# Kernel optimization log

Measured on AMD Instinct MI355X. Metric: run time of the kernel, lower is better.

The kernel has to match this reference:

```python
import jax, jax.numpy as jnp
import numpy as np

EPS = 1e-5  # torch group_norm default
GROUPS = 32


def _nin(t, W, b):
    # torch Nin: einsum('bchw,co->bowh') transposes spatial dims, then adds bias
    return jnp.einsum('bchw,co->bowh', t, W) + b


def setup_inputs() -> dict:
    key = jax.random.key(0)
    ks = jax.random.split(key, 9)
    B, C, N = 16, 512, 32
    x = jax.random.normal(ks[0], (B, C, N, N), jnp.float32)
    sc = 0.02
    Wq = jax.random.normal(ks[1], (C, C), jnp.float32) * sc
    Wk = jax.random.normal(ks[2], (C, C), jnp.float32) * sc
    Wv = jax.random.normal(ks[3], (C, C), jnp.float32) * sc
    Wn = jax.random.normal(ks[4], (C, C), jnp.float32) * sc
    bq = jnp.zeros((1, C, 1, 1), jnp.float32)
    bk = jnp.zeros((1, C, 1, 1), jnp.float32)
    bv = jnp.zeros((1, C, 1, 1), jnp.float32)
    bn = jnp.zeros((1, C, 1, 1), jnp.float32)
    return {"x": x, "Wq": Wq, "bq": bq, "Wk": Wk, "bk": bk,
            "Wv": Wv, "bv": bv, "Wn": Wn, "bn": bn}


def reference(x, Wq, bq, Wk, bk, Wv, bv, Wn, bn):
    B, C, H, W = x.shape
    # GroupNorm(32) with no affine params
    xg = x.reshape(B, GROUPS, -1)
    mu = xg.mean(-1, keepdims=True)
    var = xg.var(-1, keepdims=True)
    h = ((xg - mu) / jnp.sqrt(var + EPS)).reshape(B, C, H, W)
    # Nin projections -> spatially transposed (B, C, W, H)
    q = _nin(h, Wq, bq)
    k = _nin(h, Wk, bk)
    v = _nin(h, Wv, bv)
    # scores s[b,w1,w2,h1,h2] = sum_c q[b,c,w1,h1] k[b,c,w2,h2] * C^-0.5
    s = jnp.einsum('bcwh,bcWH->bwWhH', q, k) * (C ** -0.5)
    # softmax over flat (h1,h2) blocks exactly as the torch reshape does
    s = jax.nn.softmax(s.reshape(B, H, W, H * W), axis=-1).reshape(B, H, W, H, W)
    # torch.einsum('bHWHW, bcWH -> bcWH', w, v) takes the DIAGONAL over the
    # repeated H and W labels: diag[b,i,j] = s[b,i,j,i,j], then elementwise
    # scales v: out[b,c,w,h] = diag[b,h,w] * v[b,c,w,h]
    i = jnp.arange(H)
    j = jnp.arange(W)
    diag = s[:, i[:, None], j[None, :], i[:, None], j[None, :]]  # (B,H,W)
    h2 = v * jnp.swapaxes(diag, 1, 2)[:, None]  # (B,C,W,H)
    out = _nin(h2, Wn, bn)  # transposes back -> (B,C,H,W)
    return x + out
```

## Files before the change

### kernel.cpp

```cpp
#include <hip/hip_runtime.h>
#include <hip/hip_bf16.h>

typedef __attribute__((ext_vector_type(8))) short short8;
typedef __attribute__((ext_vector_type(4))) float floatx4;

#define MFMA16(a, b, c) __builtin_amdgcn_mfma_f32_16x16x32_bf16((a), (b), (c), 0, 0, 0)
#define WAIT_VM(N) asm volatile("s_waitcnt vmcnt(" #N ")" ::: "memory")
#define BAR() __builtin_amdgcn_s_barrier()

__device__ __forceinline__ short f2bf(float f) {
    union { float f; unsigned u; } x; x.f = f;
    unsigned r = (x.u + 0x7fffu + ((x.u >> 16) & 1u)) >> 16;
    return (short)r;
}

__device__ __forceinline__ void gl2lds16(const short* g, short* l) {
    void* gv = const_cast<short*>(g);
    __builtin_amdgcn_global_load_lds((__attribute__((address_space(1))) void*)gv,
                                     (__attribute__((address_space(3))) void*)l,
                                     16, 0, 0);
}

__global__ void transpose_w4(const float* __restrict__ Wq, const float* __restrict__ Wk,
                             const float* __restrict__ Wv, const float* __restrict__ Wn,
                             const float* __restrict__ bq, const float* __restrict__ bk,
                             const float* __restrict__ bv,
                             short* __restrict__ Wqkv_t, short* __restrict__ Wn_t,
                             float* __restrict__ bias_cat) {
    __shared__ float t[32][33];
    int z = blockIdx.z;
    const float* Wsrc = (z == 0) ? Wq : (z == 1) ? Wk : (z == 2) ? Wv : Wn;
    int o0 = blockIdx.x * 32, c0 = blockIdx.y * 32;
    int lx = threadIdx.x, ly = threadIdx.y;
    for (int i = ly; i < 32; i += 8) t[i][lx] = Wsrc[(size_t)(c0 + i) * 512 + o0 + lx];
    __syncthreads();
    for (int i = ly; i < 32; i += 8) {
        short v = f2bf(t[lx][i]);
        if (z < 3) Wqkv_t[(size_t)(z * 512 + o0 + i) * 512 + c0 + lx] = v;
        else       Wn_t[(size_t)(o0 + i) * 512 + c0 + lx] = v;
    }
    if (z < 3 && blockIdx.y == 0 && ly == 0) {
        const float* bsrc = (z == 0) ? bq : (z == 1) ? bk : bv;
        bias_cat[z * 512 + o0 + lx] = bsrc[o0 + lx];
    }
}

__global__ __launch_bounds__(256) void groupnorm_k(const float* __restrict__ x,
                                                   short* __restrict__ hnt) {
    int b = blockIdx.x >> 5, g = blockIdx.x & 31;
    const float* xg = x + ((size_t)b * 512 + g * 16) * 1024;
    const float4* xg4 = (const float4*)xg;
    float s = 0.f, ss = 0.f;
    for (int i = threadIdx.x; i < 4096; i += 256) {
        float4 v = xg4[i];
        s  += v.x + v.y + v.z + v.w;
        ss += v.x * v.x + v.y * v.y + v.z * v.z + v.w * v.w;
    }
#pragma unroll
    for (int off = 32; off > 0; off >>= 1) {
        s  += __shfl_down(s,  off, 64);
        ss += __shfl_down(ss, off, 64);
    }
    __shared__ float red[8];
    int w = threadIdx.x >> 6;
    if ((threadIdx.x & 63) == 0) { red[w] = s; red[4 + w] = ss; }
    __syncthreads();
    float S  = red[0] + red[1] + red[2] + red[3];
    float SS = red[4] + red[5] + red[6] + red[7];
    float mean = S * (1.f / 16384.f);
    float var  = SS * (1.f / 16384.f) - mean * mean;
    float rstd = rsqrtf(var + 1e-5f);
    __shared__ __attribute__((aligned(16))) short tile[16 * 1026];
    for (int i = threadIdx.x; i < 4096; i += 256) {
        float4 v = xg4[i];
        int c = i >> 8, p = (i & 255) * 4;
        short* tp = tile + c * 1026 + p;
        tp[0] = f2bf((v.x - mean) * rstd);
        tp[1] = f2bf((v.y - mean) * rstd);
        tp[2] = f2bf((v.z - mean) * rstd);
        tp[3] = f2bf((v.w - mean) * rstd);
    }
    __syncthreads();
    for (int i = threadIdx.x; i < 2048; i += 256) {
        int p = i >> 1, half = i & 1;
        short8 v;
#pragma unroll
        for (int j = 0; j < 8; ++j) v[j] = tile[(half * 8 + j) * 1026 + p];
        *(short8*)(hnt + ((size_t)b * 1024 + p) * 512 + g * 16 + half * 8) = v;
    }
}

__global__ __launch_bounds__(256) void qkv_gemm(const short* __restrict__ A,
                                                const short* __restrict__ Wt,
                                                const float* __restrict__ bias_cat,
                                                short* __restrict__ Qp,
                                                short* __restrict__ Kp,
                                                short* __restrict__ Vb) {
    const int tid = threadIdx.x;
    const int wv = tid >> 6, ln = tid & 63;
    const int fid = blockIdx.x + (blockIdx.y << 3) + blockIdx.z * 96;
    const int xcd = fid & 7, slot = fid >> 3;
    const int bb = (slot >= 96) ? 1 : 0;
    const int w = slot - bb * 96;
    const int batch = xcd * 2 + bb;
    const int m0 = (w & 7) * 128, n0 = (w >> 3) * 128;
    const size_t BS = 1024 * 512;
    const short* Ab = A + (size_t)batch * BS;
    const int tsel = n0 >> 9;
    const int permute = (tsel < 2);
    short* Ob = ((tsel == 0) ? Qp : (tsel == 1) ? Kp : Vb) + (size_t)batch * BS;

    __shared__ __attribute__((aligned(16))) short As[3][128 * 32];
    __shared__ __attribute__((aligned(16))) short Bs[3][128 * 32];

    floatx4 acc[4][4] = {};
    const int wm = (wv >> 1) * 64, wn = (wv & 1) * 64;
    const int fr = ln & 15, fq = ln >> 4;

    int sr[2], sq[2];
#pragma unroll
    for (int j = 0; j < 2; ++j) {
        int s = (wv * 2 + j) * 64 + ln;
        sr[j] = s >> 2;
        sq[j] = ((s & 3) ^ ((sr[j] >> 1) & 3)) * 8;
    }
    int aoff[4], boff[4];
#pragma unroll
    for (int t = 0; t < 4; ++t) {
        int ra = wm + t * 16 + fr;
        aoff[t] = ra * 32 + ((fq ^ ((ra >> 1) & 3)) * 8);
        int rb = wn + t * 16 + fr;
        boff[t] = rb * 32 + ((fq ^ ((rb >> 1) & 3)) * 8);
    }

    short* a0 = &As[0][0]; short* a1 = &As[1][0]; short* a2 = &As[2][0];
    short* b0 = &Bs[0][0]; short* b1 = &Bs[1][0]; short* b2 = &Bs[2][0];

#pragma unroll
    for (int j = 0; j < 2; ++j) {
        gl2lds16(Ab + (size_t)(m0 + sr[j]) * 512 + sq[j],      a0 + (wv * 2 + j) * 512);
        gl2lds16(Wt + (size_t)(n0 + sr[j]) * 512 + sq[j],      b0 + (wv * 2 + j) * 512);
        gl2lds16(Ab + (size_t)(m0 + sr[j]) * 512 + 32 + sq[j], a1 + (wv * 2 + j) * 512);
        gl2lds16(Wt + (size_t)(n0 + sr[j]) * 512 + 32 + sq[j], b1 + (wv * 2 + j) * 512);
    }

    auto compute = [&](const short* Ap, const short* Bp) {
        short8 af[4], bfr[4];
#pragma unroll
        for (int t = 0; t < 4; ++t) {
            af[t]  = *(const short8*)(Ap + aoff[t]);
            bfr[t] = *(const short8*)(Bp + boff[t]);
        }
#pragma unroll
        for (int mt = 0; mt < 4; ++mt)
#pragma unroll
            for (int nt = 0; nt < 4; ++nt)
                acc[mt][nt] = MFMA16(af[mt], bfr[nt], acc[mt][nt]);
    };

    for (int t = 0; t < 14; ++t) {
        int kp = t * 32 + 64;
#pragma unroll
        for (int j = 0; j < 2; ++j) {
            gl2lds16(Ab + (size_t)(m0 + sr[j]) * 512 + kp + sq[j], a2 + (wv * 2 + j) * 512);
            gl2lds16(Wt + (size_t)(n0 + sr[j]) * 512 + kp + sq[j], b2 + (wv * 2 + j) * 512);
        }
        WAIT_VM(8);
        BAR();
        compute(a0, b0);
        BAR();
        short* ta = a0; a0 = a1; a1 = a2; a2 = ta;
        short* tb = b0; b0 = b1; b1 = b2; b2 = tb;
    }
    WAIT_VM(4); BAR();
    compute(a0, b0);
    WAIT_VM(0); BAR();
    compute(a1, b1);

#pragma unroll
    for (int mt = 0; mt < 4; ++mt) {
#pragma unroll
        for (int nt = 0; nt < 4; ++nt) {
            int n = n0 + wn + nt * 16 + fr;
            float bvv = bias_cat[n];
            int nn = n & 511;
#pragma unroll
            for (int r = 0; r < 4; ++r) {
                int m = m0 + wm + mt * 16 + fq * 4 + r;
                int mrow = permute ? ((m & 31) * 32 + (m >> 5)) : m;
                Ob[(size_t)mrow * 512 + nn] = f2bf(acc[mt][nt][r] + bvv);
            }
        }
    }
}

__global__ __launch_bounds__(256, 2) void attn_sm(const short* __restrict__ Qp,
                                                  const short* __restrict__ Kp,
                                                  float* __restrict__ Dm) {
    const int tid = threadIdx.x;
    const int wv = tid >> 6, ln = tid & 63;
    const int fid = blockIdx.x + (blockIdx.y << 3) + blockIdx.z * 32;
    const int xcd = fid & 7, slot = fid >> 3;
    const int bb = (slot >= 32) ? 1 : 0;
    const int w = slot - bb * 32;
    const int b = xcd * 2 + bb;
    const int m0 = (w & 7) * 128, n0 = (w >> 3) * 256;
    const short* Qb = Qp + (size_t)b * (1024 * 512);
    const short* Kb = Kp + (size_t)b * (1024 * 512);

    __shared__ __attribute__((aligned(16))) short As[3][128 * 32];
    __shared__ __attribute__((aligned(16))) short Bs[3][256 * 32];

    floatx4 acc[4][8] = {};
    const int wm = (wv >> 1) * 64, wn = (wv & 1) * 128;
    const int fr = ln & 15, fq = ln >> 4;

    int ar[2], aq[2], br[4], bq_[4];
#pragma unroll
    for (int j = 0; j < 2; ++j) {
        int s = (wv * 2 + j) * 64 + ln;
        ar[j] = s >> 2;
        aq[j] = ((s & 3) ^ ((ar[j] >> 1) & 3)) * 8;
    }
#pragma unroll
    for (int j = 0; j < 4; ++j) {
        int s = (wv * 4 + j) * 64 + ln;
        br[j] = s >> 2;
        bq_[j] = ((s & 3) ^ ((br[j] >> 1) & 3)) * 8;
    }
    int aoff[4], boff[8];
#pragma unroll
    for (int t = 0; t < 4; ++t) {
        int ra = wm + t * 16 + fr;
        aoff[t] = ra * 32 + ((fq ^ ((ra >> 1) & 3)) * 8);
    }
#pragma unroll
    for (int u = 0; u < 8; ++u) {
        int rb = wn + u * 16 + fr;
        boff[u] = rb * 32 + ((fq ^ ((rb >> 1) & 3)) * 8);
    }

    short* a0 = &As[0][0]; short* a1 = &As[1][0]; short* a2 = &As[2][0];
    short* b0 = &Bs[0][0]; short* b1 = &Bs[1][0]; short* b2 = &Bs[2][0];

#pragma unroll
    for (int j = 0; j < 2; ++j) {
        gl2lds16(Qb + (size_t)(m0 + ar[j]) * 512 + aq[j],      a0 + (wv * 2 + j) * 512);
        gl2lds16(Qb + (size_t)(m0 + ar[j]) * 512 + 32 + aq[j], a1 + (wv * 2 + j) * 512);
    }
#pragma unroll
    for (int j = 0; j < 4; ++j) {
        gl2lds16(Kb + (size_t)(n0 + br[j]) * 512 + bq_[j],      b0 + (wv * 4 + j) * 512);
        gl2lds16(Kb + (size_t)(n0 + br[j]) * 512 + 32 + bq_[j], b1 + (wv * 4 + j) * 512);
    }

    auto compute = [&](const short* Ap, const short* Bp) {
        short8 af[4], bfr[8];
#pragma unroll
        for (int t = 0; t < 4; ++t) af[t] = *(const short8*)(Ap + aoff[t]);
#pragma unroll
        for (int u = 0; u < 8; ++u) bfr[u] = *(const short8*)(Bp + boff[u]);
#pragma unroll
        for (int mt = 0; mt < 4; ++mt)
#pragma unroll
            for (int nt = 0; nt < 8; ++nt)
                acc[mt][nt] = MFMA16(af[mt], bfr[nt], acc[mt][nt]);
    };

    for (int t = 0; t < 14; ++t) {
        int kp = t * 32 + 64;
#pragma unroll
        for (int j = 0; j < 2; ++j)
            gl2lds16(Qb + (size_t)(m0 + ar[j]) * 512 + kp + aq[j], a2 + (wv * 2 + j) * 512);
#pragma unroll
        for (int j = 0; j < 4; ++j)
            gl2lds16(Kb + (size_t)(n0 + br[j]) * 512 + kp + bq_[j], b2 + (wv * 4 + j) * 512);
        WAIT_VM(12);
        BAR();
        compute(a0, b0);
        BAR();
        short* ta = a0; a0 = a1; a1 = a2; a2 = ta;
        short* tb = b0; b0 = b1; b1 = b2; b2 = tb;
    }
    WAIT_VM(6); BAR();
    compute(a0, b0);
    WAIT_VM(0); BAR();
    compute(a1, b1);

    const float scale = 0.04419417382415922f;
    const int wbase = (m0 + wm) >> 5;
    const int Wbase = (n0 + wn) >> 5;
#pragma unroll
    for (int si = 0; si < 2; ++si) {
#pragma unroll
        for (int sj = 0; sj < 4; ++sj) {
            int wg = wbase + si, Wg = Wbase + sj;
            float tv[16];
            float mx = -3.0e38f;
#pragma unroll
            for (int mi = 0; mi < 2; ++mi)
#pragma unroll
                for (int ni = 0; ni < 2; ++ni)
#pragma unroll
                    for (int r = 0; r < 4; ++r) {
                        float u = acc[2 * si + mi][2 * sj + ni][r] * scale;
                        tv[(mi * 2 + ni) * 4 + r] = u;
                        mx = fmaxf(mx, u);
                    }
#pragma unroll
            for (int off = 32; off > 0; off >>= 1) mx = fmaxf(mx, __shfl_xor(mx, off, 64));
            float se = 0.f;
#pragma unroll
            for (int i = 0; i < 16; ++i) se += __expf(tv[i] - mx);
#pragma unroll
            for (int off = 32; off > 0; off >>= 1) se += __shfl_xor(se, off, 64);
            if (fq == ((wg >> 2) & 3) && fr == (Wg & 15)) {
                int mi = wg >> 4, ni = Wg >> 4;
                float numer = tv[(mi * 2 + ni) * 4 + (wg & 3)];
                Dm[((size_t)b * 32 + wg) * 32 + Wg] = __expf(numer - mx) / se;
            }
        }
    }
}

__global__ __launch_bounds__(256) void out_gemm(const short* __restrict__ A,
                                                const short* __restrict__ Wt,
                                                const float* __restrict__ Dm,
                                                const float* __restrict__ bnb,
                                                const float* __restrict__ x,
                                                float* __restrict__ out) {
    const int tid = threadIdx.x;
    const int wv = tid >> 6, ln = tid & 63;
    const int fid = blockIdx.x + (blockIdx.y << 3) + blockIdx.z * 32;
    const int xcd = fid & 7, slot = fid >> 3;
    const int bb = (slot >= 32) ? 1 : 0;
    const int w = slot - bb * 32;
    const int b = xcd * 2 + bb;
    const int m0 = (w & 7) * 128, n0 = (w >> 3) * 128;
    const size_t BS = 1024 * 512;
    const short* Ab = A + (size_t)b * BS;

    __shared__ __attribute__((aligned(16))) short As[3][128 * 32];
    __shared__ __attribute__((aligned(16))) short Bs[3][128 * 32];

    floatx4 acc[4][4] = {};
    const int wm = (wv >> 1) * 64, wn = (wv & 1) * 64;
    const int fr = ln & 15, fq = ln >> 4;

    int sr[2], sq[2];
#pragma unroll
    for (int j = 0; j < 2; ++j) {
        int s = (wv * 2 + j) * 64 + ln;
        sr[j] = s >> 2;
        sq[j] = ((s & 3) ^ ((sr[j] >> 1) & 3)) * 8;
    }
    int aoff[4], boff[4];
#pragma unroll
    for (int t = 0; t < 4; ++t) {
        int ra = wm + t * 16 + fr;
        aoff[t] = ra * 32 + ((fq ^ ((ra >> 1) & 3)) * 8);
        int rb = wn + t * 16 + fr;
        boff[t] = rb * 32 + ((fq ^ ((rb >> 1) & 3)) * 8);
    }

    short* a0 = &As[0][0]; short* a1 = &As[1][0]; short* a2 = &As[2][0];
    short* b0 = &Bs[0][0]; short* b1 = &Bs[1][0]; short* b2 = &Bs[2][0];

#pragma unroll
    for (int j = 0; j < 2; ++j) {
        gl2lds16(Ab + (size_t)(m0 + sr[j]) * 512 + sq[j],      a0 + (wv * 2 + j) * 512);
        gl2lds16(Wt + (size_t)(n0 + sr[j]) * 512 + sq[j],      b0 + (wv * 2 + j) * 512);
        gl2lds16(Ab + (size_t)(m0 + sr[j]) * 512 + 32 + sq[j], a1 + (wv * 2 + j) * 512);
        gl2lds16(Wt + (size_t)(n0 + sr[j]) * 512 + 32 + sq[j], b1 + (wv * 2 + j) * 512);
    }

    auto compute = [&](const short* Ap, const short* Bp) {
        short8 af[4], bfr[4];
#pragma unroll
        for (int t = 0; t < 4; ++t) {
            af[t]  = *(const short8*)(Ap + aoff[t]);
            bfr[t] = *(const short8*)(Bp + boff[t]);
        }
#pragma unroll
        for (int mt = 0; mt < 4; ++mt)
#pragma unroll
            for (int nt = 0; nt < 4; ++nt)
                acc[mt][nt] = MFMA16(af[mt], bfr[nt], acc[mt][nt]);
    };

    for (int t = 0; t < 14; ++t) {
        int kp = t * 32 + 64;
#pragma unroll
        for (int j = 0; j < 2; ++j) {
            gl2lds16(Ab + (size_t)(m0 + sr[j]) * 512 + kp + sq[j], a2 + (wv * 2 + j) * 512);
            gl2lds16(Wt + (size_t)(n0 + sr[j]) * 512 + kp + sq[j], b2 + (wv * 2 + j) * 512);
        }
        WAIT_VM(8);
        BAR();
        compute(a0, b0);
        BAR();
        short* ta = a0; a0 = a1; a1 = a2; a2 = ta;
        short* tb = b0; b0 = b1; b1 = b2; b2 = tb;
    }
    WAIT_VM(4); BAR();
    compute(a0, b0);
    WAIT_VM(0); BAR();
    compute(a1, b1);

#pragma unroll
    for (int mt = 0; mt < 4; ++mt) {
        int mbase = m0 + wm + mt * 16 + fq * 4;
        float4 d4 = *(const float4*)(Dm + (size_t)b * 1024 + mbase);
#pragma unroll
        for (int nt = 0; nt < 4; ++nt) {
            int n = n0 + wn + nt * 16 + fr;
            float bvv = bnb[n];
            size_t base = ((size_t)b * 512 + n) * 1024 + mbase;
            float4 x4 = *(const float4*)(x + base);
            float4 o;
            o.x = x4.x + d4.x * acc[mt][nt][0] + bvv;
            o.y = x4.y + d4.y * acc[mt][nt][1] + bvv;
            o.z = x4.z + d4.z * acc[mt][nt][2] + bvv;
            o.w = x4.w + d4.w * acc[mt][nt][3] + bvv;
            *(float4*)(out + base) = o;
        }
    }
}

extern "C" void kernel_launch(void* const* d_in, const int* in_sizes, int n_in,
                              void* d_out, int out_size, void* d_ws, size_t ws_size,
                              hipStream_t stream) {
    const float* x  = (const float*)d_in[0];
    const float* Wq = (const float*)d_in[1];
    const float* bq = (const float*)d_in[2];
    const float* Wk = (const float*)d_in[3];
    const float* bk = (const float*)d_in[4];
    const float* Wv = (const float*)d_in[5];
    const float* bv = (const float*)d_in[6];
    const float* Wn = (const float*)d_in[7];
    const float* bn = (const float*)d_in[8];
    float* out = (float*)d_out;
    char* ws = (char*)d_ws;

    const size_t WQKV = (size_t)1536 * 512 * 2;
    const size_t WSZ  = (size_t)512 * 512 * 2;
    const size_t BIAS = 1536 * sizeof(float);
    const size_t TSZ  = (size_t)16 * 1024 * 512 * 2;
    short* Wqkv_t   = (short*)(ws);
    short* Wn_t     = (short*)(ws + WQKV);
    float* bias_cat = (float*)(ws + WQKV + WSZ);
    char*  base     = ws + WQKV + WSZ + BIAS;
    short* hnt = (short*)(base);
    short* Qp  = (short*)(base + TSZ);
    short* Kp  = (short*)(base + 2 * TSZ);
    short* Vb  = (short*)(base + 3 * TSZ);
    float* Dm  = (float*)(base + 4 * TSZ);

    transpose_w4<<<dim3(16, 16, 4), dim3(32, 8), 0, stream>>>(
        Wq, Wk, Wv, Wn, bq, bk, bv, Wqkv_t, Wn_t, bias_cat);
    groupnorm_k<<<512, 256, 0, stream>>>(x, hnt);
    qkv_gemm<<<dim3(8, 12, 16), 256, 0, stream>>>(hnt, Wqkv_t, bias_cat, Qp, Kp, Vb);
    attn_sm<<<dim3(8, 4, 16), 256, 0, stream>>>(Qp, Kp, Dm);
    out_gemm<<<dim3(8, 4, 16), 256, 0, stream>>>(Vb, Wn_t, Dm, bn, x, out);
}
```

Measured before the change: 201.4 us.

## Fold Q/K and V/out projections into precomputed weight products

Replaces the three per-batch QKV projections with algebraically folded weight products: G = Wq·Wk^T so scores become h·G·h^T plus rank-one bias terms, and W2 = Wv·Wn so the output GEMM reads normalized activations directly. Bias contributions are precomputed as vectors (u, v, c, Wn^T·bv) and applied in the attention and output epilogues. This cuts the per-batch GEMM work from three projections to one and drops the Q/K/V buffers. In exchange it adds small weight-only GEMM and prep kernels plus extra bf16 rounding of the fused weight products.

```diff
diff --git a/kernel.cpp b/kernel.cpp
--- a/kernel.cpp
+++ b/kernel.cpp
@@ -13,6 +13,10 @@
     unsigned r = (x.u + 0x7fffu + ((x.u >> 16) & 1u)) >> 16;
     return (short)r;
 }
+__device__ __forceinline__ float b2f(short s) {
+    union { unsigned u; float f; } x; x.u = ((unsigned)(unsigned short)s) << 16; return x.f;
+}
+__device__ __forceinline__ int swap5(int p) { return ((p & 31) << 5) | (p >> 5); }
 
 __device__ __forceinline__ void gl2lds16(const short* g, short* l) {
     void* gv = const_cast<short*>(g);
@@ -21,28 +25,140 @@
                                      16, 0, 0);
 }
 
-__global__ void transpose_w4(const float* __restrict__ Wq, const float* __restrict__ Wk,
-                             const float* __restrict__ Wv, const float* __restrict__ Wn,
-                             const float* __restrict__ bq, const float* __restrict__ bk,
-                             const float* __restrict__ bv,
-                             short* __restrict__ Wqkv_t, short* __restrict__ Wn_t,
-                             float* __restrict__ bias_cat) {
+__global__ void prep_w(const float* __restrict__ Wq, const float* __restrict__ Wk,
+                       const float* __restrict__ Wv, const float* __restrict__ Wn,
+                       short* __restrict__ Wqc, short* __restrict__ Wkc,
+                       short* __restrict__ Wvc, short* __restrict__ Wnt) {
     __shared__ float t[32][33];
     int z = blockIdx.z;
-    const float* Wsrc = (z == 0) ? Wq : (z == 1) ? Wk : (z == 2) ? Wv : Wn;
     int o0 = blockIdx.x * 32, c0 = blockIdx.y * 32;
     int lx = threadIdx.x, ly = threadIdx.y;
-    for (int i = ly; i < 32; i += 8) t[i][lx] = Wsrc[(size_t)(c0 + i) * 512 + o0 + lx];
-    __syncthreads();
-    for (int i = ly; i < 32; i += 8) {
-        short v = f2bf(t[lx][i]);
-        if (z < 3) Wqkv_t[(size_t)(z * 512 + o0 + i) * 512 + c0 + lx] = v;
-        else       Wn_t[(size_t)(o0 + i) * 512 + c0 + lx] = v;
-    }
-    if (z < 3 && blockIdx.y == 0 && ly == 0) {
-        const float* bsrc = (z == 0) ? bq : (z == 1) ? bk : bv;
-        bias_cat[z * 512 + o0 + lx] = bsrc[o0 + lx];
-    }
+    if (z < 3) {
+        const float* src = (z == 0) ? Wq : (z == 1) ? Wk : Wv;
+        short* dst = (z == 0) ? Wqc : (z == 1) ? Wkc : Wvc;
+        for (int i = ly; i < 32; i += 8) {
+            size_t idx = (size_t)(c0 + i) * 512 + o0 + lx;
+            dst[idx] = f2bf(src[idx]);
+        }
+    } else {
+        for (int i = ly; i < 32; i += 8) t[i][lx] = Wn[(size_t)(c0 + i) * 512 + o0 + lx];
+        __syncthreads();
+        for (int i = ly; i < 32; i += 8)
+            Wnt[(size_t)(o0 + i) * 512 + c0 + lx] = f2bf(t[lx][i]);
+    }
+}
+
+__global__ void prep_uv(const float* __restrict__ Wq, const float* __restrict__ Wk,
+                        const float* __restrict__ Wn, const float* __restrict__ bq,
+                        const float* __restrict__ bk, const float* __restrict__ bv,
+                        float* __restrict__ UVC) {
+    int t = threadIdx.x;
+    float u = 0.f, v = 0.f, w2 = 0.f;
+    for (int o = 0; o < 512; ++o) {
+        u  += Wq[(size_t)t * 512 + o] * bk[o];
+        v  += Wk[(size_t)t * 512 + o] * bq[o];
+        w2 += bv[o] * Wn[(size_t)o * 512 + t];
+    }
+    UVC[t] = u; UVC[512 + t] = v; UVC[1025 + t] = w2;
+    if (t == 0) {
+        float c = 0.f;
+        for (int o = 0; o < 512; ++o) c += bq[o] * bk[o];
+        UVC[1024] = c;
+    }
+}
+
+__global__ __launch_bounds__(256) void gemm2(const short* __restrict__ Wkc,
+                                             const short* __restrict__ Wqc,
+                                             const short* __restrict__ Wnt,
+                                             const short* __restrict__ Wvc,
+                                             short* __restrict__ Gt,
+                                             short* __restrict__ W2t) {
+    const int tid = threadIdx.x;
+    const int wv = tid >> 6, ln = tid & 63;
+    const int z = blockIdx.y;
+    const short* A  = (z == 0) ? Wkc : Wnt;
+    const short* Wt = (z == 0) ? Wqc : Wvc;
+    short* O = (z == 0) ? Gt : W2t;
+    const int m0 = (blockIdx.x & 3) * 128, n0 = (blockIdx.x >> 2) * 128;
+
+    __shared__ __attribute__((aligned(16))) short As[3][128 * 32];
+    __shared__ __attribute__((aligned(16))) short Bs[3][128 * 32];
+
+    floatx4 acc[4][4] = {};
+    const int wm = (wv >> 1) * 64, wn = (wv & 1) * 64;
+    const int fr = ln & 15, fq = ln >> 4;
+
+    int sr[2], sq[2];
+#pragma unroll
+    for (int j = 0; j < 2; ++j) {
+        int s = (wv * 2 + j) * 64 + ln;
+        sr[j] = s >> 2;
+        sq[j] = ((s & 3) ^ ((sr[j] >> 1) & 3)) * 8;
+    }
+    int aoff[4], boff[4];
+#pragma unroll
+    for (int t = 0; t < 4; ++t) {
+        int ra = wm + t * 16 + fr;
+        aoff[t] = ra * 32 + ((fq ^ ((ra >> 1) & 3)) * 8);
+        int rb = wn + t * 16 + fr;
+        boff[t] = rb * 32 + ((fq ^ ((rb >> 1) & 3)) * 8);
+    }
+
+    short* a0 = &As[0][0]; short* a1 = &As[1][0]; short* a2 = &As[2][0];
+    short* b0 = &Bs[0][0]; short* b1 = &Bs[1][0]; short* b2 = &Bs[2][0];
+
+#pragma unroll
+    for (int j = 0; j < 2; ++j) {
+        gl2lds16(A  + (size_t)(m0 + sr[j]) * 512 + sq[j],      a0 + (wv * 2 + j) * 512);
+        gl2lds16(Wt + (size_t)(n0 + sr[j]) * 512 + sq[j],      b0 + (wv * 2 + j) * 512);
+        gl2lds16(A  + (size_t)(m0 + sr[j]) * 512 + 32 + sq[j], a1 + (wv * 2 + j) * 512);
+        gl2lds16(Wt + (size_t)(n0 + sr[j]) * 512 + 32 + sq[j], b1 + (wv * 2 + j) * 512);
+    }
+
+    auto compute = [&](const short* Ap, const short* Bp) {
+        short8 af[4], bfr[4];
+#pragma unroll
+        for (int t = 0; t < 4; ++t) {
+            af[t]  = *(const short8*)(Ap + aoff[t]);
+            bfr[t] = *(const short8*)(Bp + boff[t]);
+        }
+#pragma unroll
+        for (int mt = 0; mt < 4; ++mt)
+#pragma unroll
+            for (int nt = 0; nt < 4; ++nt)
+                acc[mt][nt] = MFMA16(af[mt], bfr[nt], acc[mt][nt]);
+    };
+
+    for (int t = 0; t < 14; ++t) {
+        int kp = t * 32 + 64;
+#pragma unroll
+        for (int j = 0; j < 2; ++j) {
+            gl2lds16(A  + (size_t)(m0 + sr[j]) * 512 + kp + sq[j], a2 + (wv * 2 + j) * 512);
+            gl2lds16(Wt + (size_t)(n0 + sr[j]) * 512 + kp + sq[j], b2 + (wv * 2 + j) * 512);
+        }
+        WAIT_VM(8);
+        BAR();
+        compute(a0, b0);
+        BAR();
+        short* ta = a0; a0 = a1; a1 = a2; a2 = ta;
+        short* tb = b0; b0 = b1; b1 = b2; b2 = tb;
+    }
+    WAIT_VM(4); BAR();
+    compute(a0, b0);
+    WAIT_VM(0); BAR();
+    compute(a1, b1);
+
+#pragma unroll
+    for (int mt = 0; mt < 4; ++mt)
+#pragma unroll
+        for (int nt = 0; nt < 4; ++nt) {
+            int n = n0 + wn + nt * 16 + fr;
+#pragma unroll
+            for (int r = 0; r < 4; ++r) {
+                int m = m0 + wm + mt * 16 + fq * 4 + r;
+                O[(size_t)m * 512 + n] = f2bf(acc[mt][nt][r]);
+            }
+        }
 }
 
 __global__ __launch_bounds__(256) void groupnorm_k(const float* __restrict__ x,
@@ -90,25 +206,48 @@
     }
 }
 
-__global__ __launch_bounds__(256) void qkv_gemm(const short* __restrict__ A,
-                                                const short* __restrict__ Wt,
-                                                const float* __restrict__ bias_cat,
-                                                short* __restrict__ Qp,
-                                                short* __restrict__ Kp,
-                                                short* __restrict__ Vb) {
+__global__ __launch_bounds__(256) void ruv_k(const short* __restrict__ hnt,
+                                             const float* __restrict__ UVC,
+                                             float* __restrict__ RuP,
+                                             float* __restrict__ RvP) {
+    const int b = blockIdx.x >> 4, part = blockIdx.x & 15;
+    const int wv = threadIdx.x >> 6, ln = threadIdx.x & 63;
+    float uc[8], vc[8];
+#pragma unroll
+    for (int j = 0; j < 8; ++j) { uc[j] = UVC[ln * 8 + j]; vc[j] = UVC[512 + ln * 8 + j]; }
+    for (int rr = 0; rr < 16; ++rr) {
+        int p = part * 64 + wv * 16 + rr;
+        short8 h = *(const short8*)(hnt + ((size_t)b * 1024 + p) * 512 + ln * 8);
+        float su = 0.f, sv = 0.f;
+#pragma unroll
+        for (int j = 0; j < 8; ++j) { float hv = b2f(h[j]); su += hv * uc[j]; sv += hv * vc[j]; }
+#pragma unroll
+        for (int off = 32; off > 0; off >>= 1) {
+            su += __shfl_xor(su, off, 64);
+            sv += __shfl_xor(sv, off, 64);
+        }
+        if (ln == 0) {
+            int pp = swap5(p);
+            RuP[(size_t)b * 1024 + pp] = su;
+            RvP[(size_t)b * 1024 + pp] = sv;
+        }
+    }
+}
+
+__global__ __launch_bounds__(256) void tgemm(const short* __restrict__ A,
+                                             const short* __restrict__ Gt,
+                                             short* __restrict__ Tp) {
     const int tid = threadIdx.x;
     const int wv = tid >> 6, ln = tid & 63;
-    const int fid = blockIdx.x + (blockIdx.y << 3) + blockIdx.z * 96;
+    const int fid = blockIdx.x;
     const int xcd = fid & 7, slot = fid >> 3;
-    const int bb = (slot >= 96) ? 1 : 0;
-    const int w = slot - bb * 96;
+    const int bb = (slot >= 32) ? 1 : 0;
+    const int w = slot - bb * 32;
     const int batch = xcd * 2 + bb;
     const int m0 = (w & 7) * 128, n0 = (w >> 3) * 128;
     const size_t BS = 1024 * 512;
     const short* Ab = A + (size_t)batch * BS;
-    const int tsel = n0 >> 9;
-    const int permute = (tsel < 2);
-    short* Ob = ((tsel == 0) ? Qp : (tsel == 1) ? Kp : Vb) + (size_t)batch * BS;
+    short* Ob = Tp + (size_t)batch * BS;
 
     __shared__ __attribute__((aligned(16))) short As[3][128 * 32];
     __shared__ __attribute__((aligned(16))) short Bs[3][128 * 32];
@@ -139,9 +278,9 @@
 #pragma unroll
     for (int j = 0; j < 2; ++j) {
         gl2lds16(Ab + (size_t)(m0 + sr[j]) * 512 + sq[j],      a0 + (wv * 2 + j) * 512);
-        gl2lds16(Wt + (size_t)(n0 + sr[j]) * 512 + sq[j],      b0 + (wv * 2 + j) * 512);
+        gl2lds16(Gt + (size_t)(n0 + sr[j]) * 512 + sq[j],      b0 + (wv * 2 + j) * 512);
         gl2lds16(Ab + (size_t)(m0 + sr[j]) * 512 + 32 + sq[j], a1 + (wv * 2 + j) * 512);
-        gl2lds16(Wt + (size_t)(n0 + sr[j]) * 512 + 32 + sq[j], b1 + (wv * 2 + j) * 512);
+        gl2lds16(Gt + (size_t)(n0 + sr[j]) * 512 + 32 + sq[j], b1 + (wv * 2 + j) * 512);
     }
 
     auto compute = [&](const short* Ap, const short* Bp) {
@@ -163,7 +302,7 @@
 #pragma unroll
         for (int j = 0; j < 2; ++j) {
             gl2lds16(Ab + (size_t)(m0 + sr[j]) * 512 + kp + sq[j], a2 + (wv * 2 + j) * 512);
-            gl2lds16(Wt + (size_t)(n0 + sr[j]) * 512 + kp + sq[j], b2 + (wv * 2 + j) * 512);
+            gl2lds16(Gt + (size_t)(n0 + sr[j]) * 512 + kp + sq[j], b2 + (wv * 2 + j) * 512);
         }
         WAIT_VM(8);
         BAR();
@@ -178,24 +317,23 @@
     compute(a1, b1);
 
 #pragma unroll
-    for (int mt = 0; mt < 4; ++mt) {
+    for (int mt = 0; mt < 4; ++mt)
 #pragma unroll
         for (int nt = 0; nt < 4; ++nt) {
             int n = n0 + wn + nt * 16 + fr;
-            float bvv = bias_cat[n];
-            int nn = n & 511;
 #pragma unroll
             for (int r = 0; r < 4; ++r) {
                 int m = m0 + wm + mt * 16 + fq * 4 + r;
-                int mrow = permute ? ((m & 31) * 32 + (m >> 5)) : m;
-                Ob[(size_t)mrow * 512 + nn] = f2bf(acc[mt][nt][r] + bvv);
+                Ob[(size_t)swap5(m) * 512 + n] = f2bf(acc[mt][nt][r]);
             }
         }
-    }
-}
-
-__global__ __launch_bounds__(256, 2) void attn_sm(const short* __restrict__ Qp,
-                                                  const short* __restrict__ Kp,
+}
+
+__global__ __launch_bounds__(256, 2) void attn_sm(const short* __restrict__ Tp,
+                                                  const short* __restrict__ H,
+                                                  const float* __restrict__ RuP,
+                                                  const float* __restrict__ RvP,
+                                                  const float* __restrict__ UVC,
                                                   float* __restrict__ Dm) {
     const int tid = threadIdx.x;
     const int wv = tid >> 6, ln = tid & 63;
@@ -205,8 +343,9 @@
     const int w = slot - bb * 32;
     const int b = xcd * 2 + bb;
     const int m0 = (w & 7) * 128, n0 = (w >> 3) * 256;
-    const short* Qb = Qp + (size_t)b * (1024 * 512);
-    const short* Kb = Kp + (size_t)b * (1024 * 512);
+    const size_t BS = 1024 * 512;
+    const short* Tb = Tp + (size_t)b * BS;
+    const short* Hb = H + (size_t)b * BS;
 
     __shared__ __attribute__((aligned(16))) short As[3][128 * 32];
     __shared__ __attribute__((aligned(16))) short Bs[3][256 * 32];
@@ -215,18 +354,21 @@
     const int wm = (wv >> 1) * 64, wn = (wv & 1) * 128;
     const int fr = ln & 15, fq = ln >> 4;
 
-    int ar[2], aq[2], br[4], bq_[4];
+    const short* pA[2];
+    const short* pB[4];
 #pragma unroll
     for (int j = 0; j < 2; ++j) {
         int s = (wv * 2 + j) * 64 + ln;
-        ar[j] = s >> 2;
-        aq[j] = ((s & 3) ^ ((ar[j] >> 1) & 3)) * 8;
+        int r = s >> 2;
+        int q = ((s & 3) ^ ((r >> 1) & 3)) * 8;
+        pA[j] = Tb + (size_t)(m0 + r) * 512 + q;
     }
 #pragma unroll
     for (int j = 0; j < 4; ++j) {
         int s = (wv * 4 + j) * 64 + ln;
-        br[j] = s >> 2;
-        bq_[j] = ((s & 3) ^ ((br[j] >> 1) & 3)) * 8;
+        int r = s >> 2;
+        int q = ((s & 3) ^ ((r >> 1) & 3)) * 8;
+        pB[j] = Hb + (size_t)swap5(n0 + r) * 512 + q;
     }
     int aoff[4], boff[8];
 #pragma unroll
@@ -245,13 +387,13 @@
 
 #pragma unroll
     for (int j = 0; j < 2; ++j) {
-        gl2lds16(Qb + (size_t)(m0 + ar[j]) * 512 + aq[j],      a0 + (wv * 2 + j) * 512);
-        gl2lds16(Qb + (size_t)(m0 + ar[j]) * 512 + 32 + aq[j], a1 + (wv * 2 + j) * 512);
+        gl2lds16(pA[j],      a0 + (wv * 2 + j) * 512);
+        gl2lds16(pA[j] + 32, a1 + (wv * 2 + j) * 512);
     }
 #pragma unroll
     for (int j = 0; j < 4; ++j) {
-        gl2lds16(Kb + (size_t)(n0 + br[j]) * 512 + bq_[j],      b0 + (wv * 4 + j) * 512);
-        gl2lds16(Kb + (size_t)(n0 + br[j]) * 512 + 32 + bq_[j], b1 + (wv * 4 + j) * 512);
+        gl2lds16(pB[j],      b0 + (wv * 4 + j) * 512);
+        gl2lds16(pB[j] + 32, b1 + (wv * 4 + j) * 512);
     }
 
     auto compute = [&](const short* Ap, const short* Bp) {
@@ -271,10 +413,10 @@
         int kp = t * 32 + 64;
 #pragma unroll
         for (int j = 0; j < 2; ++j)
-            gl2lds16(Qb + (size_t)(m0 + ar[j]) * 512 + kp + aq[j], a2 + (wv * 2 + j) * 512);
+            gl2lds16(pA[j] + kp, a2 + (wv * 2 + j) * 512);
 #pragma unroll
         for (int j = 0; j < 4; ++j)
-            gl2lds16(Kb + (size_t)(n0 + br[j]) * 512 + kp + bq_[j], b2 + (wv * 4 + j) * 512);
+            gl2lds16(pB[j] + kp, b2 + (wv * 4 + j) * 512);
         WAIT_VM(12);
         BAR();
         compute(a0, b0);
@@ -288,6 +430,7 @@
     compute(a1, b1);
 
     const float scale = 0.04419417382415922f;
+    const float c0v = UVC[1024];
     const int wbase = (m0 + wm) >> 5;
     const int Wbase = (n0 + wn) >> 5;
 #pragma unroll
@@ -298,15 +441,20 @@
             float tv[16];
             float mx = -3.0e38f;
 #pragma unroll
-            for (int mi = 0; mi < 2; ++mi)
-#pragma unroll
-                for (int ni = 0; ni < 2; ++ni)
+            for (int mi = 0; mi < 2; ++mi) {
+                float4 ru4 = *(const float4*)(RuP + (size_t)b * 1024 + m0 + wm + (2 * si + mi) * 16 + fq * 4);
+                const float* rup = (const float*)&ru4;
+#pragma unroll
+                for (int ni = 0; ni < 2; ++ni) {
+                    float rvv = RvP[(size_t)b * 1024 + n0 + wn + (2 * sj + ni) * 16 + fr];
 #pragma unroll
                     for (int r = 0; r < 4; ++r) {
-                        float u = acc[2 * si + mi][2 * sj + ni][r] * scale;
+                        float u = (acc[2 * si + mi][2 * sj + ni][r] + rup[r] + rvv + c0v) * scale;
                         tv[(mi * 2 + ni) * 4 + r] = u;
                         mx = fmaxf(mx, u);
                     }
+                }
+            }
 #pragma unroll
             for (int off = 32; off > 0; off >>= 1) mx = fmaxf(mx, __shfl_xor(mx, off, 64));
             float se = 0.f;
@@ -325,6 +473,7 @@
 
 __global__ __launch_bounds__(256) void out_gemm(const short* __restrict__ A,
                                                 const short* __restrict__ Wt,
+                                                const float* __restrict__ UVC,
                                                 const float* __restrict__ Dm,
                                                 const float* __restrict__ bnb,
                                                 const float* __restrict__ x,
@@ -415,13 +564,14 @@
         for (int nt = 0; nt < 4; ++nt) {
             int n = n0 + wn + nt * 16 + fr;
             float bvv = bnb[n];
+            float w2bn = UVC[1025 + n];
             size_t base = ((size_t)b * 512 + n) * 1024 + mbase;
             float4 x4 = *(const float4*)(x + base);
             float4 o;
-            o.x = x4.x + d4.x * acc[mt][nt][0] + bvv;
-            o.y = x4.y + d4.y * acc[mt][nt][1] + bvv;
-            o.z = x4.z + d4.z * acc[mt][nt][2] + bvv;
-            o.w = x4.w + d4.w * acc[mt][nt][3] + bvv;
+            o.x = x4.x + d4.x * (acc[mt][nt][0] + w2bn) + bvv;
+            o.y = x4.y + d4.y * (acc[mt][nt][1] + w2bn) + bvv;
+            o.z = x4.z + d4.z * (acc[mt][nt][2] + w2bn) + bvv;
+            o.w = x4.w + d4.w * (acc[mt][nt][3] + w2bn) + bvv;
             *(float4*)(out + base) = o;
         }
     }
@@ -442,24 +592,28 @@
     float* out = (float*)d_out;
     char* ws = (char*)d_ws;
 
-    const size_t WQKV = (size_t)1536 * 512 * 2;
-    const size_t WSZ  = (size_t)512 * 512 * 2;
-    const size_t BIAS = 1536 * sizeof(float);
-    const size_t TSZ  = (size_t)16 * 1024 * 512 * 2;
-    short* Wqkv_t   = (short*)(ws);
-    short* Wn_t     = (short*)(ws + WQKV);
-    float* bias_cat = (float*)(ws + WQKV + WSZ);
-    char*  base     = ws + WQKV + WSZ + BIAS;
-    short* hnt = (short*)(base);
-    short* Qp  = (short*)(base + TSZ);
-    short* Kp  = (short*)(base + 2 * TSZ);
-    short* Vb  = (short*)(base + 3 * TSZ);
-    float* Dm  = (float*)(base + 4 * TSZ);
-
-    transpose_w4<<<dim3(16, 16, 4), dim3(32, 8), 0, stream>>>(
-        Wq, Wk, Wv, Wn, bq, bk, bv, Wqkv_t, Wn_t, bias_cat);
+    const size_t WSZ = (size_t)512 * 512 * 2;
+    const size_t TSZ = (size_t)16 * 1024 * 512 * 2;
+    short* Wqc = (short*)(ws);
+    short* Wkc = (short*)(ws + WSZ);
+    short* Wvc = (short*)(ws + 2 * WSZ);
+    short* Wnt = (short*)(ws + 3 * WSZ);
+    short* Gt  = (short*)(ws + 4 * WSZ);
+    short* W2t = (short*)(ws + 5 * WSZ);
+    float* UVC = (float*)(ws + 6 * WSZ);
+    float* RuP = (float*)(ws + 6 * WSZ + 8192);
+    float* RvP = (float*)(ws + 6 * WSZ + 8192 + 65536);
+    float* Dm  = (float*)(ws + 6 * WSZ + 8192 + 2 * 65536);
+    char*  big = ws + 6 * WSZ + 8192 + 3 * 65536;
+    short* hnt = (short*)(big);
+    short* Tp  = (short*)(big + TSZ);
+
+    prep_w<<<dim3(16, 16, 4), dim3(32, 8), 0, stream>>>(Wq, Wk, Wv, Wn, Wqc, Wkc, Wvc, Wnt);
+    prep_uv<<<1, 512, 0, stream>>>(Wq, Wk, Wn, bq, bk, bv, UVC);
+    gemm2<<<dim3(16, 2), 256, 0, stream>>>(Wkc, Wqc, Wnt, Wvc, Gt, W2t);
     groupnorm_k<<<512, 256, 0, stream>>>(x, hnt);
-    qkv_gemm<<<dim3(8, 12, 16), 256, 0, stream>>>(hnt, Wqkv_t, bias_cat, Qp, Kp, Vb);
-    attn_sm<<<dim3(8, 4, 16), 256, 0, stream>>>(Qp, Kp, Dm);
-    out_gemm<<<dim3(8, 4, 16), 256, 0, stream>>>(Vb, Wn_t, Dm, bn, x, out);
-}
+    ruv_k<<<256, 256, 0, stream>>>(hnt, UVC, RuP, RvP);
+    tgemm<<<512, 256, 0, stream>>>(hnt, Gt, Tp);
+    attn_sm<<<dim3(8, 4, 16), 256, 0, stream>>>(Tp, hnt, RuP, RvP, UVC, Dm);
+    out_gemm<<<dim3(8, 4, 16), 256, 0, stream>>>(hnt, W2t, UVC, Dm, bn, x, out);
+}
```

Result: slower. 335.4 us (+66.6%).
